# Optimization experiments

Hardware: AMD Instinct MI355X
Metric: run time of the kernel (lower is better)

Reference implementation:

```python
import jax, jax.numpy as jnp
import numpy as np

IN_CH = 64
OUT_CH = 64
K = 5
PAD = 2
B, H, W = 16, 128, 128


def _build_buffers():
    # Mirrors the torch __init__ geometry construction exactly.
    r = (K - 1) // 2
    x = np.arange(-r, r + 1)
    X = np.stack(np.meshgrid(x, x, indexing='ij'), -1).astype(np.float32)  # (K,K,2)
    R = np.sqrt((X ** 2).sum(-1))                                          # (K,K)
    with np.errstate(divide='ignore', invalid='ignore'):
        Xhat = X / R[..., None]
    Xhat[R == 0] = 0.0
    Xhat = np.transpose(Xhat, (2, 0, 1))                 # (2,K,K)
    XX = Xhat[None, :] * Xhat[:, None]                   # (2,2,K,K) outer product
    XX = np.tile(XX, (OUT_CH, IN_CH, 1, 1))              # (2*out, 2*in, K, K)
    rs, inds = np.unique(R, return_inverse=True)
    inds = inds.reshape(K, K).astype(np.int32)
    indsxx = inds - 1
    indsxx[indsxx == -1] = 0                              # r=0 bin has no xx term (masked by XX=0 there)
    identity = np.tile(np.eye(2, dtype=np.float32), (OUT_CH, IN_CH))[..., None, None]  # (2*out,2*in,1,1)
    return XX.astype(np.float32), identity, indsxx, inds, len(rs)


def setup_inputs() -> dict:
    XX, identity, indsxx, indsid, L = _build_buffers()
    key = jax.random.key(0)
    k1, k2, k3 = jax.random.split(key, 3)
    scale = np.float32(1.0 / np.sqrt(3 * IN_CH * 2))
    return {
        'x': jax.random.normal(k1, (B, 2 * IN_CH, H, W), jnp.float32),
        'weightsxx': jax.random.normal(k2, (OUT_CH, IN_CH, L - 1), jnp.float32) * scale,
        'weightsidentity': jax.random.normal(k3, (OUT_CH, IN_CH, L), jnp.float32) * scale,
        'XhatXhat': jnp.asarray(XX),
        'identity': jnp.asarray(identity),
        'indsxx': jnp.asarray(indsxx),
        'indsidentity': jnp.asarray(indsid),
        'padding': PAD,
    }


def _build_kernel(weightsxx, weightsidentity, XhatXhat, identity, indsxx, indsidentity):
    # repeat_interleave(.,2,axis) == jnp.repeat(.,2,axis); then radial gather over (K,K)
    cxx = jnp.repeat(jnp.repeat(weightsxx, 2, axis=0), 2, axis=1)[..., indsxx] * XhatXhat
    cid = jnp.repeat(jnp.repeat(weightsidentity, 2, axis=0), 2, axis=1)[..., indsidentity] * identity
    return cxx + cid  # (2*out, 2*in, K, K)


def reference(x, weightsxx, weightsidentity, XhatXhat, identity, indsxx, indsidentity, padding):
    c = _build_kernel(weightsxx, weightsidentity, XhatXhat, identity, indsxx, indsidentity)
    xp = jnp.pad(x, ((0, 0), (0, 0), (padding, padding), (padding, padding)))
    return jax.lax.conv_general_dilated(
        xp, c, window_strides=(1, 1), padding='VALID',
        dimension_numbers=('NCHW', 'OIHW', 'NCHW'))
```

## Files before the change

kernel.cpp:

```cpp
#include <hip/hip_runtime.h>
#include <hip/hip_bf16.h>
#include <utility>

typedef __bf16        bf16x8 __attribute__((ext_vector_type(8)));
typedef float         f32x16 __attribute__((ext_vector_type(16)));
typedef unsigned int  u32x4  __attribute__((ext_vector_type(4)));
typedef unsigned int   u32;
typedef unsigned short u16;

template<int N> using IC = std::integral_constant<int, N>;

__device__ __forceinline__ u16 f32_to_bf16(float f) {
    u32 u = __builtin_bit_cast(u32, f);
    u = (u + 0x7FFFu + ((u >> 16) & 1u)) >> 16;
    return (u16)u;
}
__device__ __forceinline__ u32 pack2bf(float a, float b) {
    return (u32)f32_to_bf16(a) | ((u32)f32_to_bf16(b) << 16);
}

__global__ void build_c(const float* __restrict__ wxx,
                        const float* __restrict__ wid,
                        const float* __restrict__ XX,
                        const float* __restrict__ ident,
                        const int*   __restrict__ indsxx,
                        const int*   __restrict__ indsid,
                        u16*         __restrict__ cb)
{
    int idx = blockIdx.x * 256 + threadIdx.x;
    if (idx >= 25 * 128 * 128) return;
    int b = idx & 127;
    int a = (idx >> 7) & 127;
    int t = idx >> 14;
    int w2 = (a >> 1) * 64 + (b >> 1);
    float v = wxx[w2 * 5 + indsxx[t]] * XX[(a * 128 + b) * 25 + t]
            + ident[a * 128 + b]      * wid[w2 * 6 + indsid[t]];
    cb[idx] = f32_to_bf16(v);
}

constexpr int LDSROW = 128 * 48;
constexpr int LDSBUF = 8 * LDSROW;
constexpr int ZOFF   = 2 * LDSBUF;

__global__ void __launch_bounds__(512, 1)
conv_mfma(const float* __restrict__ x,
          const u16*   __restrict__ cb,
          float*       __restrict__ out)
{
    __shared__ unsigned char lds[2 * LDSBUF + 16];

    const int tid    = threadIdx.x;
    const int lane   = tid & 63;
    const int wv     = tid >> 6;
    const int wave_m = wv & 1;
    const int wave_q = wv >> 1;
    const int l31    = lane & 31;
    const int h2     = lane >> 5;

    const int bid  = blockIdx.x;
    const int sbid = (bid & 7) * 64 + (bid >> 3);
    const int bb   = sbid >> 5;
    const int h0   = (sbid & 31) << 2;

    const int wc  = tid & 127;
    const int ic8 = (tid >> 7) & 1;
    const int rh  = tid >> 8;

    if (tid < 4) *reinterpret_cast<u32*>(&lds[ZOFF + tid * 4]) = 0u;

    f32x16 acc[2][4];
    #pragma unroll
    for (int i = 0; i < 2; ++i)
        #pragma unroll
        for (int j = 0; j < 4; ++j)
            #pragma unroll
            for (int k = 0; k < 16; ++k) acc[i][j][k] = 0.f;

    float pf[4][8];

    const float* xbase = x + (size_t)bb * (128 * 16384) + wc;
    const u16*   cbA0  = cb + (wave_m * 64 + l31) * 128 + h2 * 8;
    const int    wpx_b = wave_q * 32 + l31 - 2;

    auto ISSUE = [&](auto Uc, int s) {
        constexpr int U = decltype(Uc)::value;
        const int hp = h0 - 2 + 2 * U + rh;
        if ((unsigned)hp < 128u) {
            const float* px = xbase + (size_t)(s * 16 + ic8 * 8) * 16384 + hp * 128;
            #pragma unroll
            for (int j = 0; j < 8; ++j) pf[U][j] = px[(size_t)j * 16384];
        } else {
            #pragma unroll
            for (int j = 0; j < 8; ++j) pf[U][j] = 0.f;
        }
    };

    auto WRITE = [&](auto Uc, int wbuf) {
        constexpr int U = decltype(Uc)::value;
        u32x4 v;
        v[0] = pack2bf(pf[U][0], pf[U][1]);
        v[1] = pack2bf(pf[U][2], pf[U][3]);
        v[2] = pack2bf(pf[U][4], pf[U][5]);
        v[3] = pack2bf(pf[U][6], pf[U][7]);
        *reinterpret_cast<u32x4*>(&lds[wbuf * LDSBUF + (2 * U + rh) * LDSROW
                                       + wc * 48 + ic8 * 16]) = v;
    };

    auto CLUSTER = [&](auto KWc, int s) {
        constexpr int KW = decltype(KWc)::value;
        const u16* abase = cbA0 + KW * 16384 + s * 16;
        bf16x8 A[5][2];
        #pragma unroll
        for (int kh = 0; kh < 5; ++kh) {
            A[kh][0] = *reinterpret_cast<const bf16x8*>(abase + kh * 81920);
            A[kh][1] = *reinterpret_cast<const bf16x8*>(abase + kh * 81920 + 4096);
        }
        const int wpx  = wpx_b + KW;
        const bool vld = (unsigned)wpx < 128u;
        const unsigned char* lbase = vld ? &lds[(s & 1) * LDSBUF + wpx * 48 + h2 * 16]
                                         : &lds[ZOFF];
        const int rstep = vld ? LDSROW : 0;
        __builtin_amdgcn_s_setprio(1);
        #pragma unroll
        for (int rp = 0; rp < 8; ++rp) {
            const bf16x8 b = *reinterpret_cast<const bf16x8*>(lbase + rp * rstep);
            #pragma unroll
            for (int kh = 0; kh < 5; ++kh) {
                const int n = rp - kh;
                if (0 <= n && n < 4) {
                    acc[0][n] = __builtin_amdgcn_mfma_f32_32x32x16_bf16(A[kh][0], b, acc[0][n], 0, 0, 0);
                    acc[1][n] = __builtin_amdgcn_mfma_f32_32x32x16_bf16(A[kh][1], b, acc[1][n], 0, 0, 0);
                }
            }
        }
        __builtin_amdgcn_s_setprio(0);
    };

    ISSUE(IC<0>{}, 0); ISSUE(IC<1>{}, 0); ISSUE(IC<2>{}, 0); ISSUE(IC<3>{}, 0);
    WRITE(IC<0>{}, 0); WRITE(IC<1>{}, 0); WRITE(IC<2>{}, 0); WRITE(IC<3>{}, 0);
    __syncthreads();

    #pragma unroll 1
    for (int s = 0; s < 8; ++s) {
        const int nb = (s + 1) & 1;
        if (s < 7) {
            ISSUE(IC<0>{}, s + 1); ISSUE(IC<1>{}, s + 1);
            ISSUE(IC<2>{}, s + 1); ISSUE(IC<3>{}, s + 1);
        }
        CLUSTER(IC<0>{}, s);
        if (s < 7) WRITE(IC<0>{}, nb);
        CLUSTER(IC<1>{}, s);
        if (s < 7) WRITE(IC<1>{}, nb);
        CLUSTER(IC<2>{}, s);
        if (s < 7) WRITE(IC<2>{}, nb);
        CLUSTER(IC<3>{}, s);
        if (s < 7) WRITE(IC<3>{}, nb);
        CLUSTER(IC<4>{}, s);
        __syncthreads();
    }

    const int wpix = wave_q * 32 + l31;
    #pragma unroll
    for (int m = 0; m < 2; ++m)
        #pragma unroll
        for (int reg = 0; reg < 16; ++reg) {
            const int oc = wave_m * 64 + m * 32 + (reg & 3) + ((reg >> 2) << 3) + (h2 << 2);
            float* op = out + ((size_t)(bb * 128 + oc) * 128 + h0) * 128 + wpix;
            #pragma unroll
            for (int n = 0; n < 4; ++n)
                op[n * 128] = acc[m][n][reg];
        }
}

extern "C" void kernel_launch(void* const* d_in, const int* in_sizes, int n_in,
                              void* d_out, int out_size, void* d_ws, size_t ws_size,
                              hipStream_t stream)
{
    const float* x    = (const float*)d_in[0];
    const float* wxx  = (const float*)d_in[1];
    const float* wi   = (const float*)d_in[2];
    const float* XX   = (const float*)d_in[3];
    const float* iden = (const float*)d_in[4];
    const int*   ixx  = (const int*)d_in[5];
    const int*   iid  = (const int*)d_in[6];

    u16* cbuf = (u16*)d_ws;

    build_c<<<1600, 256, 0, stream>>>(wxx, wi, XX, iden, ixx, iid, cbuf);
    conv_mfma<<<512, 512, 0, stream>>>(x, cbuf, (float*)d_out);
}
```

Measured before the change: 248.6 us.

## Split conv tile along width with explicit halo columns and two blocks per CU

Each block now covers a 64-wide half of the image row instead of the full 128 columns, so the grid doubles to 1024 blocks of 256 threads with launch bounds allowing two blocks per CU. The LDS row shrinks to 68 columns, and a small set of threads loads the 2-column halo on each side, zero-filled at image borders. That replaces the per-lane validity check and the zero-pad LDS slot in the inner loop. The aim is better occupancy and overlap between the two resident blocks. The cost is reloading halo columns and reading the weight matrix A twice as often in total, since each block reuses it over half as many pixels.

Measured after the change: 245.9 us. About the same (-1.1%).

```diff
diff --git a/kernel.cpp b/kernel.cpp
--- a/kernel.cpp
+++ b/kernel.cpp
@@ -38,16 +38,15 @@
     cb[idx] = f32_to_bf16(v);
 }
 
-constexpr int LDSROW = 128 * 48;
+constexpr int LDSROW = 68 * 48;
 constexpr int LDSBUF = 8 * LDSROW;
-constexpr int ZOFF   = 2 * LDSBUF;
-
-__global__ void __launch_bounds__(512, 1)
+
+__global__ void __launch_bounds__(256, 2)
 conv_mfma(const float* __restrict__ x,
           const u16*   __restrict__ cb,
           float*       __restrict__ out)
 {
-    __shared__ unsigned char lds[2 * LDSBUF + 16];
+    __shared__ unsigned char lds[2 * LDSBUF];
 
     const int tid    = threadIdx.x;
     const int lane   = tid & 63;
@@ -58,15 +57,21 @@
     const int h2     = lane >> 5;
 
     const int bid  = blockIdx.x;
-    const int sbid = (bid & 7) * 64 + (bid >> 3);
-    const int bb   = sbid >> 5;
-    const int h0   = (sbid & 31) << 2;
-
-    const int wc  = tid & 127;
-    const int ic8 = (tid >> 7) & 1;
-    const int rh  = tid >> 8;
-
-    if (tid < 4) *reinterpret_cast<u32*>(&lds[ZOFF + tid * 4]) = 0u;
+    const int sbid = (bid & 7) * 128 + (bid >> 3);
+    const int bb   = sbid >> 6;
+    const int tile = sbid & 63;
+    const int h0   = (tile >> 1) << 2;
+    const int w0   = (tile & 1) << 6;
+
+    const int wc  = tid & 63;
+    const int ic8 = (tid >> 6) & 1;
+    const int rh  = tid >> 7;
+
+    const int hsel  = tid & 3;
+    const int wcolH = (hsel < 2) ? (hsel - 2) : (62 + hsel);
+    const int ic8H  = (tid >> 2) & 1;
+    const int rH    = tid >> 3;
+    const int hIdxH = wcolH + 2;
 
     f32x16 acc[2][4];
     #pragma unroll
@@ -77,21 +82,36 @@
             for (int k = 0; k < 16; ++k) acc[i][j][k] = 0.f;
 
     float pf[4][8];
-
-    const float* xbase = x + (size_t)bb * (128 * 16384) + wc;
+    float pfh[8];
+
+    const float* xbase = x + (size_t)bb * (128 * 16384);
     const u16*   cbA0  = cb + (wave_m * 64 + l31) * 128 + h2 * 8;
-    const int    wpx_b = wave_q * 32 + l31 - 2;
 
     auto ISSUE = [&](auto Uc, int s) {
         constexpr int U = decltype(Uc)::value;
         const int hp = h0 - 2 + 2 * U + rh;
         if ((unsigned)hp < 128u) {
-            const float* px = xbase + (size_t)(s * 16 + ic8 * 8) * 16384 + hp * 128;
+            const float* px = xbase + (size_t)(s * 16 + ic8 * 8) * 16384 + hp * 128 + w0 + wc;
             #pragma unroll
             for (int j = 0; j < 8; ++j) pf[U][j] = px[(size_t)j * 16384];
         } else {
             #pragma unroll
             for (int j = 0; j < 8; ++j) pf[U][j] = 0.f;
+        }
+    };
+
+    auto ISSUEH = [&](int s) {
+        if (tid < 64) {
+            const int hp = h0 - 2 + rH;
+            const int gc = w0 + wcolH;
+            if ((unsigned)hp < 128u && (unsigned)gc < 128u) {
+                const float* px = xbase + (size_t)(s * 16 + ic8H * 8) * 16384 + hp * 128 + gc;
+                #pragma unroll
+                for (int j = 0; j < 8; ++j) pfh[j] = px[(size_t)j * 16384];
+            } else {
+                #pragma unroll
+                for (int j = 0; j < 8; ++j) pfh[j] = 0.f;
+            }
         }
     };
 
@@ -103,7 +123,19 @@
         v[2] = pack2bf(pf[U][4], pf[U][5]);
         v[3] = pack2bf(pf[U][6], pf[U][7]);
         *reinterpret_cast<u32x4*>(&lds[wbuf * LDSBUF + (2 * U + rh) * LDSROW
-                                       + wc * 48 + ic8 * 16]) = v;
+                                       + (wc + 2) * 48 + ic8 * 16]) = v;
+    };
+
+    auto WRITEH = [&](int wbuf) {
+        if (tid < 64) {
+            u32x4 v;
+            v[0] = pack2bf(pfh[0], pfh[1]);
+            v[1] = pack2bf(pfh[2], pfh[3]);
+            v[2] = pack2bf(pfh[4], pfh[5]);
+            v[3] = pack2bf(pfh[6], pfh[7]);
+            *reinterpret_cast<u32x4*>(&lds[wbuf * LDSBUF + rH * LDSROW
+                                           + hIdxH * 48 + ic8H * 16]) = v;
+        }
     };
 
     auto CLUSTER = [&](auto KWc, int s) {
@@ -115,15 +147,12 @@
             A[kh][0] = *reinterpret_cast<const bf16x8*>(abase + kh * 81920);
             A[kh][1] = *reinterpret_cast<const bf16x8*>(abase + kh * 81920 + 4096);
         }
-        const int wpx  = wpx_b + KW;
-        const bool vld = (unsigned)wpx < 128u;
-        const unsigned char* lbase = vld ? &lds[(s & 1) * LDSBUF + wpx * 48 + h2 * 16]
-                                         : &lds[ZOFF];
-        const int rstep = vld ? LDSROW : 0;
+        const unsigned char* lbase = &lds[(s & 1) * LDSBUF
+                                          + (wave_q * 32 + l31 + KW) * 48 + h2 * 16];
         __builtin_amdgcn_s_setprio(1);
         #pragma unroll
         for (int rp = 0; rp < 8; ++rp) {
-            const bf16x8 b = *reinterpret_cast<const bf16x8*>(lbase + rp * rstep);
+            const bf16x8 b = *reinterpret_cast<const bf16x8*>(lbase + rp * LDSROW);
             #pragma unroll
             for (int kh = 0; kh < 5; ++kh) {
                 const int n = rp - kh;
@@ -136,8 +165,8 @@
         __builtin_amdgcn_s_setprio(0);
     };
 
-    ISSUE(IC<0>{}, 0); ISSUE(IC<1>{}, 0); ISSUE(IC<2>{}, 0); ISSUE(IC<3>{}, 0);
-    WRITE(IC<0>{}, 0); WRITE(IC<1>{}, 0); WRITE(IC<2>{}, 0); WRITE(IC<3>{}, 0);
+    ISSUE(IC<0>{}, 0); ISSUE(IC<1>{}, 0); ISSUE(IC<2>{}, 0); ISSUE(IC<3>{}, 0); ISSUEH(0);
+    WRITE(IC<0>{}, 0); WRITE(IC<1>{}, 0); WRITE(IC<2>{}, 0); WRITE(IC<3>{}, 0); WRITEH(0);
     __syncthreads();
 
     #pragma unroll 1
@@ -145,7 +174,7 @@
         const int nb = (s + 1) & 1;
         if (s < 7) {
             ISSUE(IC<0>{}, s + 1); ISSUE(IC<1>{}, s + 1);
-            ISSUE(IC<2>{}, s + 1); ISSUE(IC<3>{}, s + 1);
+            ISSUE(IC<2>{}, s + 1); ISSUE(IC<3>{}, s + 1); ISSUEH(s + 1);
         }
         CLUSTER(IC<0>{}, s);
         if (s < 7) WRITE(IC<0>{}, nb);
@@ -154,12 +183,12 @@
         CLUSTER(IC<2>{}, s);
         if (s < 7) WRITE(IC<2>{}, nb);
         CLUSTER(IC<3>{}, s);
-        if (s < 7) WRITE(IC<3>{}, nb);
+        if (s < 7) { WRITE(IC<3>{}, nb); WRITEH(nb); }
         CLUSTER(IC<4>{}, s);
         __syncthreads();
     }
 
-    const int wpix = wave_q * 32 + l31;
+    const int wpix = w0 + wave_q * 32 + l31;
     #pragma unroll
     for (int m = 0; m < 2; ++m)
         #pragma unroll
@@ -187,5 +216,5 @@
     u16* cbuf = (u16*)d_ws;
 
     build_c<<<1600, 256, 0, stream>>>(wxx, wi, XX, iden, ixx, iid, cbuf);
-    conv_mfma<<<512, 512, 0, stream>>>(x, cbuf, (float*)d_out);
-}
+    conv_mfma<<<1024, 256, 0, stream>>>(x, cbuf, (float*)d_out);
+}
```
